# Kernel optimization log

Hardware: AMD Instinct MI355X
Metric: run time of the kernel (lower is better)

## Reference

```python
import jax, jax.numpy as jnp
import numpy as np

RADIUS = 0.1
NSAMPLE = 32


def ball_query(xyz, new_xyz, radius, nsample):
    """xyz:(B,N,3), new_xyz:(B,P,3) -> idx:(B,P,nsample) int32.
    Semantics of PointNet++ CUDA ball_query: first `nsample` points (in index
    order) within `radius`; remaining slots padded with the first found index
    (0 if no point is within radius)."""
    d2 = jnp.sum((new_xyz[:, :, None, :] - xyz[:, None, :, :]) ** 2, axis=-1)  # (B,P,N)
    mask = d2 < radius * radius
    cnt = jnp.cumsum(mask, axis=-1) - 1               # rank of each hit
    valid = mask & (cnt < nsample)
    first = jnp.argmax(mask, axis=-1)                 # first in-ball index (0 if none)
    B, P, N = d2.shape
    pos = jnp.where(valid, cnt, nsample)              # invalid -> dump slot
    buf = jnp.broadcast_to(first[..., None], (B, P, nsample + 1))
    j = jnp.broadcast_to(jnp.arange(N)[None, None, :], (B, P, N))
    b = jnp.arange(B)[:, None, None]
    p = jnp.arange(P)[None, :, None]
    buf = buf.at[b, p, pos].set(j)
    return buf[..., :nsample].astype(jnp.int32)


def setup_inputs() -> dict:
    key = jax.random.key(0)
    k1, k2, k3 = jax.random.split(key, 3)
    xyz = jax.random.uniform(k1, (2, 16384, 3), dtype=jnp.float32)
    new_xyz = jax.random.uniform(k2, (2, 4096, 3), dtype=jnp.float32)
    features = jax.random.normal(k3, (2, 64, 16384), dtype=jnp.float32)
    return {"xyz": xyz, "new_xyz": new_xyz, "features": features}


def reference(xyz, new_xyz, features):
    idx = ball_query(xyz, new_xyz, RADIUS, NSAMPLE)              # (B,P,S)
    grouped_xyz = jax.vmap(lambda x, i: x[i])(xyz, idx)          # (B,P,S,3)
    grouped_xyz = jnp.transpose(grouped_xyz, (0, 3, 1, 2))       # (B,3,P,S)
    grouped_xyz = grouped_xyz - jnp.transpose(new_xyz, (0, 2, 1))[..., None]
    grouped_feat = jax.vmap(lambda f, i: f[:, i])(features, idx) # (B,C,P,S)
    return jnp.concatenate([grouped_xyz, grouped_feat], axis=1)  # (B,3+C,P,S)
```

## Files before the change

### kernel.cpp

```cpp
#include <hip/hip_runtime.h>
#include <hip/hip_bf16.h>
#include <climits>

#define BATCH   2
#define NPTS    16384
#define NQ      4096
#define CFEAT   64
#define NS      32
#define R2      0.01f
#define COUT    (3 + CFEAT)
#define GDIM    10
#define NCELL   (GDIM * GDIM * GDIM)
#define NWORDS  (NPTS / 32)

#define FEATT_BYTES ((size_t)BATCH * NPTS * CFEAT * sizeof(float))
#define PXYZJ_BYTES ((size_t)BATCH * NPTS * sizeof(float4))
#define OFF_CNT    0
#define OFF_FILL   (2 * NCELL)
#define OFF_CSTART (4 * NCELL)
#define GRID_INTS  (4 * NCELL + 2 * (NCELL + 1))

__device__ __forceinline__ int cell_of(float x, float y, float z) {
    int cx = (int)(x * GDIM); cx = cx < 0 ? 0 : (cx > GDIM - 1 ? GDIM - 1 : cx);
    int cy = (int)(y * GDIM); cy = cy < 0 ? 0 : (cy > GDIM - 1 ? GDIM - 1 : cy);
    int cz = (int)(z * GDIM); cz = cz < 0 ? 0 : (cz > GDIM - 1 ? GDIM - 1 : cz);
    return (cz * GDIM + cy) * GDIM + cx;
}

__global__ __launch_bounds__(256) void prep1_kernel(
    const float* __restrict__ feat, float* __restrict__ featT,
    const float* __restrict__ xyz, int* __restrict__ cnt)
{
    __shared__ float tile[64][65];
    if (blockIdx.x < 512) {
        const int b    = blockIdx.x >> 8;
        const int n0   = (blockIdx.x & 255) * 64;
        const int lane = threadIdx.x & 63;
        const int grp  = threadIdx.x >> 6;
        const float* fb = feat + (size_t)b * CFEAT * NPTS;
        #pragma unroll
        for (int k = 0; k < 16; ++k) {
            const int c = grp * 16 + k;
            tile[c][lane] = fb[(size_t)c * NPTS + n0 + lane];
        }
        __syncthreads();
        float* db = featT + ((size_t)b * NPTS + n0) * CFEAT;
        #pragma unroll
        for (int k = 0; k < 16; ++k) {
            const int n = grp * 16 + k;
            db[(size_t)n * CFEAT + lane] = tile[lane][n];
        }
    } else {
        const int g = (blockIdx.x - 512) * 256 + threadIdx.x;
        const int b = g >> 14;
        const int c = cell_of(xyz[g*3], xyz[g*3+1], xyz[g*3+2]);
        atomicAdd(&cnt[b * NCELL + c], 1);
    }
}

__global__ __launch_bounds__(256) void prep2_kernel(
    const float* __restrict__ xyz, const int* __restrict__ cnt,
    int* __restrict__ fill, int* __restrict__ cstart,
    float4* __restrict__ pxyzj)
{
    __shared__ int scs[2 * NCELL];
    const int tid  = threadIdx.x;
    const int lane = tid & 63;

    if (tid < 128) {
        const int b = tid >> 6;
        int c16[16];
        int tot = 0;
        #pragma unroll
        for (int k = 0; k < 16; ++k) {
            const int i = lane * 16 + k;
            c16[k] = (i < NCELL) ? cnt[b * NCELL + i] : 0;
            tot += c16[k];
        }
        int ex = tot;
        #pragma unroll
        for (int off = 1; off < 64; off <<= 1) {
            const int u = __shfl_up(ex, off);
            if (lane >= off) ex += u;
        }
        ex -= tot;
        int run = ex;
        #pragma unroll
        for (int k = 0; k < 16; ++k) {
            const int i = lane * 16 + k;
            if (i < NCELL) scs[b * NCELL + i] = run;
            run += c16[k];
        }
    }
    __syncthreads();

    if (blockIdx.x == 0) {
        for (int i = tid; i < 2 * (NCELL + 1); i += 256) {
            const int b  = i / (NCELL + 1);
            const int ci = i - b * (NCELL + 1);
            cstart[i] = (ci == NCELL) ? NPTS : scs[b * NCELL + ci];
        }
    }

    const int g = blockIdx.x * 256 + tid;
    const int b = g >> 14;
    const int j = g & (NPTS - 1);
    const float x = xyz[g*3], y = xyz[g*3+1], z = xyz[g*3+2];
    const int c = cell_of(x, y, z);
    const int pos = atomicAdd(&fill[b * NCELL + c], 1);
    pxyzj[b * NPTS + scs[b * NCELL + c] + pos] =
        make_float4(x, y, z, __int_as_float(j));
}

__global__ __launch_bounds__(256) void qg_fused(
    const float* __restrict__ xyz,
    const float* __restrict__ new_xyz,
    const int* __restrict__ cstart,
    const float4* __restrict__ pxyzj,
    const float4* __restrict__ featT4,
    float* __restrict__ out)
{
    const int q    = blockIdx.x;
    const int b    = q >> 12;
    const int p    = q & (NQ - 1);
    const int tid  = threadIdx.x;
    const int wave = tid >> 6;
    const int lane = tid & 63;

    __shared__ unsigned int hmask[NWORDS];
    __shared__ int idx_s[NS];
    __shared__ float tile[NS][65];

    if (tid < 128) {
        uint4 z; z.x = 0; z.y = 0; z.z = 0; z.w = 0;
        ((uint4*)hmask)[tid] = z;
    }

    const float qx = new_xyz[q * 3 + 0];
    const float qy = new_xyz[q * 3 + 1];
    const float qz = new_xyz[q * 3 + 2];
    const float* xb = xyz + (size_t)b * NPTS * 3;
    const int* cs = cstart + b * (NCELL + 1);
    const float4* pb = pxyzj + (size_t)b * NPTS;

    int qcx = (int)(qx * GDIM); qcx = qcx < 0 ? 0 : (qcx > GDIM-1 ? GDIM-1 : qcx);
    int qcy = (int)(qy * GDIM); qcy = qcy < 0 ? 0 : (qcy > GDIM-1 ? GDIM-1 : qcy);
    int qcz = (int)(qz * GDIM); qcz = qcz < 0 ? 0 : (qcz > GDIM-1 ? GDIM-1 : qcz);
    const int x0 = qcx > 0 ? qcx - 1 : 0;
    const int x1 = qcx < GDIM-1 ? qcx + 1 : GDIM-1;
    const int y0 = qcy > 0 ? qcy - 1 : 0;
    const int y1 = qcy < GDIM-1 ? qcy + 1 : GDIM-1;
    const int z0 = qcz > 0 ? qcz - 1 : 0;
    const int z1 = qcz < GDIM-1 ? qcz + 1 : GDIM-1;
    const int ny  = y1 - y0 + 1;
    const int nyz = ny * (z1 - z0 + 1);

    int sv = 0, ev = 0;
    if (lane < nyz) {
        const int gzi = (ny == 3) ? ((lane * 86) >> 8) : (lane >> 1);
        const int gyi = lane - gzi * ny;
        const int crow = ((z0 + gzi) * GDIM + (y0 + gyi)) * GDIM;
        sv = cs[crow + x0];
        ev = cs[crow + x1 + 1];
    }
    __syncthreads();

    for (int r = wave; r < nyz; r += 4) {
        const int s = __shfl(sv, r);
        const int e = __shfl(ev, r);
        for (int pos = s; pos < e; pos += 64) {
            const int i = pos + lane;
            const bool inr = i < e;
            const float4 pt = pb[inr ? i : 0];
            const float dx = pt.x - qx;
            const float dy = pt.y - qy;
            const float dz = pt.z - qz;
            if (inr && (dx*dx + dy*dy + dz*dz < R2)) {
                const int j = __float_as_int(pt.w);
                atomicOr(&hmask[j >> 5], 1u << (j & 31));
            }
        }
    }
    __syncthreads();

    if (wave == 0) {
        unsigned int w[8];
        {
            const uint4 a = ((const uint4*)hmask)[lane * 2];
            const uint4 c = ((const uint4*)hmask)[lane * 2 + 1];
            w[0] = a.x; w[1] = a.y; w[2] = a.z; w[3] = a.w;
            w[4] = c.x; w[5] = c.y; w[6] = c.z; w[7] = c.w;
        }
        int cnt8 = 0;
        #pragma unroll
        for (int k = 0; k < 8; ++k) cnt8 += __popc(w[k]);

        int pfx = cnt8;
        #pragma unroll
        for (int off = 1; off < 64; off <<= 1) {
            const int u = __shfl_up(pfx, off);
            if (lane >= off) pfx += u;
        }
        const int K = __shfl(pfx, 63);
        pfx -= cnt8;

        if (pfx < NS && cnt8 > 0) {
            int r = pfx;
            #pragma unroll
            for (int k = 0; k < 8; ++k) {
                unsigned int m = w[k];
                while (m && r < NS) {
                    const int bit = __builtin_ctz(m);
                    idx_s[r] = lane * 256 + k * 32 + bit;
                    m &= m - 1;
                    ++r;
                }
            }
        }
        __builtin_amdgcn_wave_barrier();
        if (lane < NS && lane >= K) {
            idx_s[lane] = (K > 0) ? idx_s[0] : 0;
        }
    }
    __syncthreads();

    const int sm = tid >> 3;
    const int q8 = tid & 7;
    const float4* base = featT4 + ((size_t)b * NPTS + idx_s[sm]) * 16;
    const float4 v0 = base[q8];
    const float4 v1 = base[8 + q8];

    const size_t cstride = (size_t)NQ * NS;
    const size_t out_q   = ((size_t)b * COUT * NQ + (size_t)p) * NS;

    float xv = 0.f, yv = 0.f, zv = 0.f;
    if (tid < NS) {
        const int j = idx_s[tid];
        xv = xb[j*3+0] - qx;
        yv = xb[j*3+1] - qy;
        zv = xb[j*3+2] - qz;
    }

    ((float4*)&tile[sm][q8 * 4])[0]      = v0;
    ((float4*)&tile[sm][32 + q8 * 4])[0] = v1;

    if (tid < NS) {
        out[out_q + 0*cstride + tid] = xv;
        out[out_q + 1*cstride + tid] = yv;
        out[out_q + 2*cstride + tid] = zv;
    }
    __syncthreads();

    const int s  = tid & 31;
    const int c8 = tid >> 5;
    float* ob = out + out_q + s + 3 * cstride;
    #pragma unroll
    for (int k = 0; k < 8; ++k) {
        const int c = c8 + k * 8;
        ob[(size_t)c * cstride] = tile[s][c];
    }
}

__global__ __launch_bounds__(256) void qg_linear(
    const float* __restrict__ xyz, const float* __restrict__ new_xyz,
    const float* __restrict__ feat, float* __restrict__ out)
{
    const int wave = threadIdx.x >> 6;
    const int lane = threadIdx.x & 63;
    const int bp   = blockIdx.x * 4 + wave;
    const int b    = bp >> 12;
    const int p    = bp & (NQ - 1);
    __shared__ int idx_s[4][NS];
    const float qx = new_xyz[bp*3+0], qy = new_xyz[bp*3+1], qz = new_xyz[bp*3+2];
    const float* xb = xyz + (size_t)b * NPTS * 3;
    int cnt = 0;
    const unsigned long long below = (1ull << lane) - 1ull;
    for (int base = 0; base < NPTS; base += 64) {
        const int j = base + lane;
        const float dx = xb[j*3+0]-qx, dy = xb[j*3+1]-qy, dz = xb[j*3+2]-qz;
        const bool hit = dx*dx+dy*dy+dz*dz < R2;
        const unsigned long long m = __ballot(hit);
        if (hit) {
            const int slot = cnt + __popcll(m & below);
            if (slot < NS) idx_s[wave][slot] = j;
        }
        cnt += __popcll(m);
        if (cnt >= NS) break;
    }
    __builtin_amdgcn_wave_barrier();
    if (cnt < NS) {
        const int first = (cnt > 0) ? idx_s[wave][0] : 0;
        if (lane >= cnt && lane < NS) idx_s[wave][lane] = first;
    }
    __builtin_amdgcn_wave_barrier();
    const size_t cstride = (size_t)NQ * NS;
    const size_t out_q = ((size_t)b * COUT * NQ + (size_t)p) * NS;
    if (lane < NS) {
        const int j = idx_s[wave][lane];
        out[out_q + 0*cstride + lane] = xb[j*3+0] - qx;
        out[out_q + 1*cstride + lane] = xb[j*3+1] - qy;
        out[out_q + 2*cstride + lane] = xb[j*3+2] - qz;
    }
    const float* fb = feat + (size_t)b * CFEAT * NPTS;
    const int s = lane & 31, half = lane >> 5;
    const int j = idx_s[wave][s];
    #pragma unroll 8
    for (int c = half; c < CFEAT; c += 2)
        out[out_q + (size_t)(3 + c) * cstride + s] = fb[(size_t)c * NPTS + j];
}

extern "C" void kernel_launch(void* const* d_in, const int* in_sizes, int n_in,
                              void* d_out, int out_size, void* d_ws, size_t ws_size,
                              hipStream_t stream) {
    const float* xyz     = (const float*)d_in[0];
    const float* new_xyz = (const float*)d_in[1];
    const float* feat    = (const float*)d_in[2];
    float* out = (float*)d_out;

    const size_t need_full = FEATT_BYTES + PXYZJ_BYTES + (size_t)GRID_INTS * sizeof(int);

    if (ws_size >= need_full) {
        float*  featT = (float*)d_ws;
        float4* pxyzj = (float4*)((char*)d_ws + FEATT_BYTES);
        int* gi = (int*)((char*)d_ws + FEATT_BYTES + PXYZJ_BYTES);
        int* cnt    = gi + OFF_CNT;
        int* fill   = gi + OFF_FILL;
        int* cstart = gi + OFF_CSTART;

        hipMemsetAsync(cnt, 0, 4 * NCELL * sizeof(int), stream);
        prep1_kernel<<<512 + (BATCH * NPTS) / 256, 256, 0, stream>>>(feat, featT, xyz, cnt);
        prep2_kernel<<<(BATCH * NPTS) / 256, 256, 0, stream>>>(xyz, cnt, fill, cstart, pxyzj);
        qg_fused<<<BATCH * NQ, 256, 0, stream>>>(
            xyz, new_xyz, cstart, pxyzj, (const float4*)featT, out);
    } else {
        qg_linear<<<(BATCH * NQ) / 4, 256, 0, stream>>>(xyz, new_xyz, feat, out);
    }
}
```

Measured before the change: 119.7 us.

## Store transposed features as bf16 and compute neighbor indices redundantly per wave

The transposed feature copy is now stored as bf16 instead of fp32. This halves the bytes written by the prep kernel and the bytes gathered per neighbor in the fused kernel, with values widened back to fp32 before the output is written. In addition, every wave now runs the bitmask prefix and index extraction itself, so a block-wide barrier is replaced by a wave barrier. The cost is bf16 rounding of the output features, which may exceed a strict tolerance, plus redundant scan work and benign duplicate writes to shared memory.

```diff
diff --git a/kernel.cpp b/kernel.cpp
--- a/kernel.cpp
+++ b/kernel.cpp
@@ -13,7 +13,7 @@
 #define NCELL   (GDIM * GDIM * GDIM)
 #define NWORDS  (NPTS / 32)
 
-#define FEATT_BYTES ((size_t)BATCH * NPTS * CFEAT * sizeof(float))
+#define FEATT_BYTES ((size_t)BATCH * NPTS * CFEAT * sizeof(unsigned short))
 #define PXYZJ_BYTES ((size_t)BATCH * NPTS * sizeof(float4))
 #define OFF_CNT    0
 #define OFF_FILL   (2 * NCELL)
@@ -27,8 +27,15 @@
     return (cz * GDIM + cy) * GDIM + cx;
 }
 
+__device__ __forceinline__ unsigned short f2bf(float f) {
+    unsigned b = __float_as_uint(f);
+    return (unsigned short)((b + 0x7FFFu + ((b >> 16) & 1u)) >> 16);
+}
+__device__ __forceinline__ float bflo(unsigned u) { return __uint_as_float(u << 16); }
+__device__ __forceinline__ float bfhi(unsigned u) { return __uint_as_float(u & 0xFFFF0000u); }
+
 __global__ __launch_bounds__(256) void prep1_kernel(
-    const float* __restrict__ feat, float* __restrict__ featT,
+    const float* __restrict__ feat, unsigned short* __restrict__ featT16,
     const float* __restrict__ xyz, int* __restrict__ cnt)
 {
     __shared__ float tile[64][65];
@@ -44,11 +51,16 @@
             tile[c][lane] = fb[(size_t)c * NPTS + n0 + lane];
         }
         __syncthreads();
-        float* db = featT + ((size_t)b * NPTS + n0) * CFEAT;
-        #pragma unroll
-        for (int k = 0; k < 16; ++k) {
-            const int n = grp * 16 + k;
-            db[(size_t)n * CFEAT + lane] = tile[lane][n];
+        unsigned short* db = featT16 + ((size_t)b * NPTS + n0) * CFEAT;
+        #pragma unroll
+        for (int k = 0; k < 8; ++k) {
+            const int e   = threadIdx.x + 256 * k;
+            const int row = e >> 5;
+            const int c2  = e & 31;
+            ushort2 v;
+            v.x = f2bf(tile[2 * c2][row]);
+            v.y = f2bf(tile[2 * c2 + 1][row]);
+            ((ushort2*)(db + (size_t)row * CFEAT))[c2] = v;
         }
     } else {
         const int g = (blockIdx.x - 512) * 256 + threadIdx.x;
@@ -117,7 +129,7 @@
     const float* __restrict__ new_xyz,
     const int* __restrict__ cstart,
     const float4* __restrict__ pxyzj,
-    const float4* __restrict__ featT4,
+    const unsigned short* __restrict__ featT16,
     float* __restrict__ out)
 {
     const int q    = blockIdx.x;
@@ -183,14 +195,13 @@
     }
     __syncthreads();
 
-    if (wave == 0) {
+    {
         unsigned int w[8];
-        {
-            const uint4 a = ((const uint4*)hmask)[lane * 2];
-            const uint4 c = ((const uint4*)hmask)[lane * 2 + 1];
-            w[0] = a.x; w[1] = a.y; w[2] = a.z; w[3] = a.w;
-            w[4] = c.x; w[5] = c.y; w[6] = c.z; w[7] = c.w;
-        }
+        const uint4 a = ((const uint4*)hmask)[lane * 2];
+        const uint4 c = ((const uint4*)hmask)[lane * 2 + 1];
+        w[0] = a.x; w[1] = a.y; w[2] = a.z; w[3] = a.w;
+        w[4] = c.x; w[5] = c.y; w[6] = c.z; w[7] = c.w;
+
         int cnt8 = 0;
         #pragma unroll
         for (int k = 0; k < 8; ++k) cnt8 += __popc(w[k]);
@@ -221,14 +232,13 @@
         if (lane < NS && lane >= K) {
             idx_s[lane] = (K > 0) ? idx_s[0] : 0;
         }
-    }
-    __syncthreads();
+        __builtin_amdgcn_wave_barrier();
+    }
 
     const int sm = tid >> 3;
     const int q8 = tid & 7;
-    const float4* base = featT4 + ((size_t)b * NPTS + idx_s[sm]) * 16;
-    const float4 v0 = base[q8];
-    const float4 v1 = base[8 + q8];
+    const unsigned short* base16 = featT16 + ((size_t)b * NPTS + idx_s[sm]) * CFEAT;
+    const uint4 v = ((const uint4*)base16)[q8];
 
     const size_t cstride = (size_t)NQ * NS;
     const size_t out_q   = ((size_t)b * COUT * NQ + (size_t)p) * NS;
@@ -241,8 +251,11 @@
         zv = xb[j*3+2] - qz;
     }
 
-    ((float4*)&tile[sm][q8 * 4])[0]      = v0;
-    ((float4*)&tile[sm][32 + q8 * 4])[0] = v1;
+    float4 lo, hi;
+    lo.x = bflo(v.x); lo.y = bfhi(v.x); lo.z = bflo(v.y); lo.w = bfhi(v.y);
+    hi.x = bflo(v.z); hi.y = bfhi(v.z); hi.z = bflo(v.w); hi.w = bfhi(v.w);
+    ((float4*)&tile[sm][q8 * 8])[0]     = lo;
+    ((float4*)&tile[sm][q8 * 8 + 4])[0] = hi;
 
     if (tid < NS) {
         out[out_q + 0*cstride + tid] = xv;
@@ -320,7 +333,7 @@
     const size_t need_full = FEATT_BYTES + PXYZJ_BYTES + (size_t)GRID_INTS * sizeof(int);
 
     if (ws_size >= need_full) {
-        float*  featT = (float*)d_ws;
+        unsigned short* featT16 = (unsigned short*)d_ws;
         float4* pxyzj = (float4*)((char*)d_ws + FEATT_BYTES);
         int* gi = (int*)((char*)d_ws + FEATT_BYTES + PXYZJ_BYTES);
         int* cnt    = gi + OFF_CNT;
@@ -328,10 +341,10 @@
         int* cstart = gi + OFF_CSTART;
 
         hipMemsetAsync(cnt, 0, 4 * NCELL * sizeof(int), stream);
-        prep1_kernel<<<512 + (BATCH * NPTS) / 256, 256, 0, stream>>>(feat, featT, xyz, cnt);
+        prep1_kernel<<<512 + (BATCH * NPTS) / 256, 256, 0, stream>>>(feat, featT16, xyz, cnt);
         prep2_kernel<<<(BATCH * NPTS) / 256, 256, 0, stream>>>(xyz, cnt, fill, cstart, pxyzj);
         qg_fused<<<BATCH * NQ, 256, 0, stream>>>(
-            xyz, new_xyz, cstart, pxyzj, (const float4*)featT, out);
+            xyz, new_xyz, cstart, pxyzj, featT16, out);
     } else {
         qg_linear<<<(BATCH * NQ) / 4, 256, 0, stream>>>(xyz, new_xyz, feat, out);
     }
```

New measurement: 117.1 us. -2.2%, faster.
